# Kernel optimization log

Measured on AMD Instinct MI355X. Metric: run time of the kernel, lower is better.

Reference implementation:

```python
import jax, jax.numpy as jnp
import numpy as np

BLOCK_SIZE = 32
# E2M1 (FP4) representable magnitudes and rounding midpoints
FP4_GRID = jnp.array([0.0, 0.5, 1.0, 1.5, 2.0, 3.0, 4.0, 6.0], dtype=jnp.float32)
FP4_MIDS = jnp.array([0.25, 0.75, 1.25, 1.75, 2.5, 3.5, 5.0], dtype=jnp.float32)


def quantize_to_mxfp4(w, block_size=BLOCK_SIZE):
    """Quantize (K, N) weight to MXFP4: per-block-of-32 (along K) power-of-2 scale
    + E2M1 codes. Returns dequantized-code tensor q (K//bs, bs, N) and scales
    (K//bs, 1, N) so that dequant = q * scales."""
    K, N = w.shape
    wb = w.reshape(K // block_size, block_size, N)
    amax = jnp.max(jnp.abs(wb), axis=1, keepdims=True)          # (K//bs, 1, N)
    # E8M0 scale: 2^(floor(log2(amax)) - 2) so amax/scale falls in [4, 8) -> clipped to 6
    exp = jnp.floor(jnp.log2(jnp.maximum(amax, 1e-30))) - 2.0
    scales = jnp.exp2(exp)
    x = wb / scales
    idx = jnp.digitize(jnp.abs(x), FP4_MIDS)                    # round-to-nearest FP4 magnitude
    q = jnp.sign(x) * FP4_GRID[idx]
    return q, scales


def mxfp4_matmul(inputs, q, scales, block_size=BLOCK_SIZE):
    """inputs: (..., K); q: (K//bs, bs, N); scales: (K//bs, 1, N)."""
    K = inputs.shape[-1]
    N = q.shape[-1]
    w = (q * scales).reshape(K, N)   # fused dequant (reference form)
    return inputs @ w


def setup_inputs() -> dict:
    key = jax.random.key(0)
    ks = jax.random.split(key, 3)
    B, S, D, F = 4, 2048, 2048, 8192
    inputs = jax.random.normal(ks[0], (B, S, D), dtype=jnp.float32)
    up_kernel = jax.random.normal(ks[1], (D, F), dtype=jnp.float32) * (1.0 / np.sqrt(D))
    down_kernel = jax.random.normal(ks[2], (F, D), dtype=jnp.float32) * (1.0 / np.sqrt(F))
    up_bias = jnp.zeros((F,), dtype=jnp.float32)
    down_bias = jnp.zeros((D,), dtype=jnp.float32)
    return {"inputs": inputs, "up_kernel": up_kernel, "up_bias": up_bias,
            "down_kernel": down_kernel, "down_bias": down_bias}


def reference(inputs, up_kernel, up_bias, down_kernel, down_bias):
    q_up, s_up = quantize_to_mxfp4(up_kernel, BLOCK_SIZE)
    x = mxfp4_matmul(inputs, q_up, s_up, BLOCK_SIZE) + up_bias
    x = jax.nn.gelu(x)
    q_dn, s_dn = quantize_to_mxfp4(down_kernel, BLOCK_SIZE)
    x = mxfp4_matmul(x, q_dn, s_dn, BLOCK_SIZE) + down_bias
    return x
```

## Files before the change

### kernel.cpp

```cpp
#include <hip/hip_runtime.h>
#include <hip/hip_bf16.h>

typedef __bf16 bf16_t;
typedef __attribute__((ext_vector_type(8))) __bf16 bf16x8;
typedef __attribute__((ext_vector_type(4))) float f32x4;
typedef __attribute__((ext_vector_type(4))) unsigned int u32x4;

__device__ __forceinline__ void gload_lds16(const bf16_t* g, bf16_t* l) {
    __builtin_amdgcn_global_load_lds(
        (const __attribute__((address_space(1))) void*)g,
        (__attribute__((address_space(3))) void*)l,
        16, 0, 0);
}

__device__ __forceinline__ float gelu_f(float v) {
    float u = 0.7978845608028654f * (v + 0.044715f * v * v * v);
    float e = __expf(-2.f * u);
    float t = __fdividef(1.f - e, 1.f + e);
    return 0.5f * v * (1.f + t);
}

__device__ __forceinline__ void quant_one(const float* __restrict__ w,
                                          bf16_t* __restrict__ wt,
                                          int K, int N, int tix) {
    int n = tix % N;
    int b = tix / N;
    const float* src = w + (size_t)b * 32 * N + n;
    float v[32];
    float amax = 0.f;
#pragma unroll
    for (int i = 0; i < 32; ++i) {
        v[i] = __builtin_nontemporal_load(src + (size_t)i * N);
        amax = fmaxf(amax, fabsf(v[i]));
    }
    unsigned eb = (__float_as_uint(amax) >> 23) & 0xFF;
    float scale = __uint_as_float((eb - 2u) << 23);
    float inv   = __uint_as_float((256u - eb) << 23);
    if (amax == 0.f) { scale = 0.f; inv = 0.f; }
    bf16_t dq[32];
#pragma unroll
    for (int i = 0; i < 32; ++i) {
        float x  = v[i] * inv;
        float ax = fabsf(x);
        float q = ax < 0.25f ? 0.0f : ax < 0.75f ? 0.5f : ax < 1.25f ? 1.0f :
                  ax < 1.75f ? 1.5f : ax < 2.5f  ? 2.0f : ax < 3.5f  ? 3.0f :
                  ax < 5.0f  ? 4.0f : 6.0f;
        float d = copysignf(q * scale, x);
        dq[i] = (bf16_t)d;
    }
    const int r  = n & 255, rt = n >> 8, kt = b >> 1, ub = (b & 1) * 4;
    bf16_t* base = wt + (((size_t)rt * (K >> 6) + kt) << 14) + (r << 6);
#pragma unroll
    for (int j = 0; j < 4; ++j) {
        bf16x8 p;
#pragma unroll
        for (int t = 0; t < 8; ++t) p[t] = dq[j * 8 + t];
        *(bf16x8*)(base + (((ub + j) ^ (r & 7)) << 3)) = p;
    }
}

__global__ void prep_kernel(const float* __restrict__ in, bf16_t* __restrict__ out,
                            int ncvt, int cvtB, int dLog,
                            const float* __restrict__ upw, bf16_t* __restrict__ upwt,
                            int upK, int upN, int qupB,
                            const float* __restrict__ dnw, bf16_t* __restrict__ dnwt,
                            int dnK, int dnN) {
    int bid = blockIdx.x;
    if (bid < cvtB) {
        int i = (bid * blockDim.x + threadIdx.x) << 3;
        if (i >= ncvt) return;
        const f32x4* p = (const f32x4*)(in + i);
        f32x4 a = __builtin_nontemporal_load(p);
        f32x4 b = __builtin_nontemporal_load(p + 1);
        bf16x8 o;
        o[0] = (bf16_t)a[0]; o[1] = (bf16_t)a[1]; o[2] = (bf16_t)a[2]; o[3] = (bf16_t)a[3];
        o[4] = (bf16_t)b[0]; o[5] = (bf16_t)b[1]; o[6] = (bf16_t)b[2]; o[7] = (bf16_t)b[3];
        const int row = i >> dLog, d = i & ((1 << dLog) - 1);
        const int r = row & 255, mt = row >> 8, dt = d >> 6, u = (d >> 3) & 7;
        size_t off = (((size_t)mt * (1 << (dLog - 6)) + dt) << 14) + (r << 6)
                     + ((u ^ (r & 7)) << 3);
        *(bf16x8*)(out + off) = o;
    } else if (bid < cvtB + qupB) {
        int tix = (bid - cvtB) * blockDim.x + threadIdx.x;
        if (tix >= (upK >> 5) * upN) return;
        quant_one(upw, upwt, upK, upN, tix);
    } else {
        int tix = (bid - cvtB - qupB) * blockDim.x + threadIdx.x;
        if (tix >= (dnK >> 5) * dnN) return;
        quant_one(dnw, dnwt, dnK, dnN, tix);
    }
}

#define VMW4  asm volatile("s_waitcnt vmcnt(4)" ::: "memory")
#define VMW0  asm volatile("s_waitcnt vmcnt(0)" ::: "memory")
#define BARR  asm volatile("s_barrier" ::: "memory")
#define LGKM0 asm volatile("s_waitcnt lgkmcnt(0)" ::: "memory")

__global__ __launch_bounds__(512, 4)
void gemm1_kernel(const bf16_t* __restrict__ A, const bf16_t* __restrict__ Bt,
                  const float* __restrict__ bias, bf16_t* __restrict__ C,
                  int M, int N, int K) {
    __shared__ __align__(16) char smem[81920];
    bf16_t* sAp = (bf16_t*)smem;
    bf16_t* sBp = (bf16_t*)(smem + 65536);
    const int tid     = threadIdx.x;
    const int lane    = tid & 63;
    const int wv      = tid >> 6;
    const int wr      = wv >> 1;
    const int wc      = wv & 1;
    const int laneLow = lane & 15;
    const int laneHi  = lane >> 4;

    const int bid = blockIdx.x;
    const int xcd = bid & 7, l = bid >> 3, r = l >> 5, u = l & 31;
    const int bm = ((xcd & 1) << 3) + (u >> 2) + ((r & 1) << 4);
    const int bn = ((xcd >> 1) << 2) + (u & 3) + ((r >> 1) << 4);

    const int kT = K >> 6;
    const int rtB = bn >> 1;
    const size_t bHalf = (size_t)(bn & 1) << 13;

    auto stageA = [&](int buf, int kt) {
        const bf16_t* s = A + (((size_t)bm * kT + kt) << 14)
                            + ((wv * 8) << 6) + lane * 8;
        bf16_t* d = sAp + buf * 16384;
#pragma unroll
        for (int h = 0; h < 2; ++h) {
            gload_lds16(s + h * 8192,        d + (h * 128 + wv * 8) * 64);
            gload_lds16(s + h * 8192 + 4096, d + (h * 128 + 64 + wv * 8) * 64);
        }
    };
    auto stageB = [&](int kt) {
        const bf16_t* s = Bt + (((size_t)rtB * kT + kt) << 14) + bHalf
                             + ((wv * 8) << 6) + lane * 8;
        gload_lds16(s,        &sBp[(wv * 8) * 64]);
        gload_lds16(s + 4096, &sBp[(64 + wv * 8) * 64]);
    };

    const int s7  = laneLow & 7;
    const int xk0 = ((laneHi) ^ s7) << 3;
    const int xk1 = ((4 + laneHi) ^ s7) << 3;
    const int aOffBase = (wr * 64 + laneLow) * 64;
    const int bOffBase = (wc * 64 + laneLow) * 64;

    f32x4 acc[4][4];
#pragma unroll
    for (int i = 0; i < 4; ++i)
#pragma unroll
        for (int j = 0; j < 4; ++j) acc[i][j] = (f32x4){0.f, 0.f, 0.f, 0.f};

    stageA(0, 0);
    stageB(0);
    int cur = 0;

#pragma unroll 1
    for (int kt = 0; kt < kT; ++kt) {
        const bool nl = (kt + 1 < kT);
        if (nl) stageA(cur ^ 1, kt + 1);
        if (nl) { VMW4; } else { VMW0; }
        BARR;
        __builtin_amdgcn_s_setprio(1);
        const bf16_t* sAc = sAp + cur * 16384;
#pragma unroll
        for (int ks = 0; ks < 2; ++ks) {
            const int xk = ks ? xk1 : xk0;
            bf16x8 b0 = *(const bf16x8*)(&sBp[bOffBase + 0 * 1024 + xk]);
            bf16x8 b1 = *(const bf16x8*)(&sBp[bOffBase + 1 * 1024 + xk]);
            bf16x8 b2 = *(const bf16x8*)(&sBp[bOffBase + 2 * 1024 + xk]);
            bf16x8 b3 = *(const bf16x8*)(&sBp[bOffBase + 3 * 1024 + xk]);
#pragma unroll
            for (int m = 0; m < 4; ++m) {
                bf16x8 a = *(const bf16x8*)(&sAc[aOffBase + m * 1024 + xk]);
                acc[m][0] = __builtin_amdgcn_mfma_f32_16x16x32_bf16(a, b0, acc[m][0], 0, 0, 0);
                acc[m][1] = __builtin_amdgcn_mfma_f32_16x16x32_bf16(a, b1, acc[m][1], 0, 0, 0);
                acc[m][2] = __builtin_amdgcn_mfma_f32_16x16x32_bf16(a, b2, acc[m][2], 0, 0, 0);
                acc[m][3] = __builtin_amdgcn_mfma_f32_16x16x32_bf16(a, b3, acc[m][3], 0, 0, 0);
            }
        }
        __builtin_amdgcn_s_setprio(0);
        BARR;
        if (nl) stageB(kt + 1);
        cur ^= 1;
    }

    char* sC = smem;
#pragma unroll
    for (int n = 0; n < 4; ++n) {
        const int colL = wc * 64 + n * 16 + laneLow;
        const float bv = bias[bn * 128 + colL];
        const int u6   = (colL >> 3) & 7;
#pragma unroll
        for (int m = 0; m < 4; ++m) {
#pragma unroll
            for (int j = 0; j < 4; ++j) {
                const int rowL = wr * 64 + m * 16 + (laneHi << 2) + j;
                float v = acc[m][n][j] + bv;
                int byte = ((colL >> 6) << 15) + (rowL << 7)
                         + ((u6 ^ (rowL & 7)) << 4) + ((colL & 7) << 1);
                byte ^= ((rowL >> 2) & 3) << 5;
                *(bf16_t*)(sC + byte) = (bf16_t)gelu_f(v);
            }
        }
    }
    LGKM0;
    BARR;
    char* dst = (char*)C + (((size_t)bm * (N >> 6) + bn * 2) << 15);
#pragma unroll
    for (int s = 0; s < 8; ++s) {
        int lin = s * 8192 + tid * 16;
        int row = (lin >> 7) & 255;
        int rb  = lin ^ (((row >> 2) & 3) << 5);
        u32x4 v = *(const u32x4*)(sC + rb);
        __builtin_nontemporal_store(v, (u32x4*)(dst + lin));
    }
}

#define MFMA_ROW(MI, A0, A1)                                                          \
    acc[MI][0] = __builtin_amdgcn_mfma_f32_16x16x32_bf16(A0, bf00, acc[MI][0],0,0,0); \
    acc[MI][0] = __builtin_amdgcn_mfma_f32_16x16x32_bf16(A1, bf01, acc[MI][0],0,0,0); \
    acc[MI][1] = __builtin_amdgcn_mfma_f32_16x16x32_bf16(A0, bf10, acc[MI][1],0,0,0); \
    acc[MI][1] = __builtin_amdgcn_mfma_f32_16x16x32_bf16(A1, bf11, acc[MI][1],0,0,0); \
    acc[MI][2] = __builtin_amdgcn_mfma_f32_16x16x32_bf16(A0, bf20, acc[MI][2],0,0,0); \
    acc[MI][2] = __builtin_amdgcn_mfma_f32_16x16x32_bf16(A1, bf21, acc[MI][2],0,0,0); \
    acc[MI][3] = __builtin_amdgcn_mfma_f32_16x16x32_bf16(A0, bf30, acc[MI][3],0,0,0); \
    acc[MI][3] = __builtin_amdgcn_mfma_f32_16x16x32_bf16(A1, bf31, acc[MI][3],0,0,0);

#define PHASE(BUF, P, STAGE_STMT, TAIL_STMT)                                          \
  {                                                                                   \
    af00 = lda(BUF, 2*(P),   0); af01 = lda(BUF, 2*(P),   1);                         \
    af10 = lda(BUF, 2*(P)+1, 0); af11 = lda(BUF, 2*(P)+1, 1);                         \
    if ((P) == 0) {                                                                   \
      bf00 = ldb(BUF,0,0); bf01 = ldb(BUF,0,1);                                       \
      bf10 = ldb(BUF,1,0); bf11 = ldb(BUF,1,1);                                       \
      bf20 = ldb(BUF,2,0); bf21 = ldb(BUF,2,1);                                       \
      bf30 = ldb(BUF,3,0); bf31 = ldb(BUF,3,1);                                       \
    }                                                                                 \
    STAGE_STMT;                                                                       \
    BARR;                                                                             \
    LGKM0;                                                                            \
    __builtin_amdgcn_s_setprio(1);                                                    \
    MFMA_ROW(2*(P),   af00, af01);                                                    \
    MFMA_ROW(2*(P)+1, af10, af11);                                                    \
    __builtin_amdgcn_s_setprio(0);                                                    \
    TAIL_STMT;                                                                        \
    BARR;                                                                             \
  }

__global__ __launch_bounds__(512, 2)
void gemm2_kernel(const bf16_t* __restrict__ A, const bf16_t* __restrict__ Bt,
                  const float* __restrict__ bias, float* __restrict__ Cf,
                  int M, int N, int K) {
    __shared__ __align__(16) char smem[131072];
    bf16_t* sAp = (bf16_t*)smem;
    bf16_t* sBp = (bf16_t*)(smem + 65536);
    const int tid     = threadIdx.x;
    const int lane    = tid & 63;
    const int wv      = tid >> 6;
    const int wr      = wv >> 2;
    const int wc      = wv & 3;
    const int laneLow = lane & 15;
    const int laneHi  = lane >> 4;

    const int ntn = N >> 8;
    const int nwg = gridDim.x;
    const int bid = blockIdx.x;
    int wg  = (bid & 7) * (nwg >> 3) + (bid >> 3);
    const int bm = wg / ntn, bn = wg % ntn;

    const int kT = K >> 6;

    auto stageA = [&](int b, int kt, int h) {
        const bf16_t* s = A + (((size_t)bm * kT + kt) << 14)
                            + ((h * 128 + wv * 8) << 6) + lane * 8;
        gload_lds16(s,        &sAp[b * 16384 + (h * 128 + wv * 8) * 64]);
        gload_lds16(s + 4096, &sAp[b * 16384 + (h * 128 + 64 + wv * 8) * 64]);
    };
    auto stageB = [&](int b, int kt, int h) {
        const bf16_t* s = Bt + (((size_t)bn * kT + kt) << 14)
                             + ((h * 128 + wv * 8) << 6) + lane * 8;
        gload_lds16(s,        &sBp[b * 16384 + (h * 128 + wv * 8) * 64]);
        gload_lds16(s + 4096, &sBp[b * 16384 + (h * 128 + 64 + wv * 8) * 64]);
    };

    const int s7  = laneLow & 7;
    const int xk0 = ((laneHi) ^ s7) << 3;
    const int xk1 = ((4 + laneHi) ^ s7) << 3;
    const int aOffBase = (wr * 128 + laneLow) * 64;
    const int bOffBase = (wc * 64 + laneLow) * 64;
    auto lda = [&](int b, int m, int ks) -> bf16x8 {
        return *(const bf16x8*)(&sAp[b * 16384 + aOffBase + m * 1024 + (ks ? xk1 : xk0)]);
    };
    auto ldb = [&](int b, int n2, int ks) -> bf16x8 {
        return *(const bf16x8*)(&sBp[b * 16384 + bOffBase + n2 * 1024 + (ks ? xk1 : xk0)]);
    };

    f32x4 acc[8][4];
#pragma unroll
    for (int i = 0; i < 8; ++i)
#pragma unroll
        for (int j = 0; j < 4; ++j) acc[i][j] = (f32x4){0.f, 0.f, 0.f, 0.f};

    bf16x8 af00, af01, af10, af11;
    bf16x8 bf00, bf01, bf10, bf11, bf20, bf21, bf30, bf31;

    stageA(0, 0, 0); stageA(0, 0, 1);
    stageB(0, 0, 0); stageB(0, 0, 1);
    stageB(1, 1, 0); stageB(1, 1, 1);
    VMW4;
    BARR;

    const int niter = kT >> 1;
    for (int i = 0; i < niter; ++i) {
        const bool nlast = (i + 1 < niter);
        const int kO  = 2 * i + 1;
        const int kN  = 2 * i + 2;
        const int kN1 = 2 * i + 3;
        PHASE(0, 0, stageA(1, kO, 0), ((void)0));
        PHASE(0, 1, stageA(1, kO, 1), ((void)0));
        PHASE(0, 2, if (nlast) stageB(0, kN, 0), ((void)0));
        PHASE(0, 3, if (nlast) stageB(0, kN, 1),
              if (nlast) { VMW4; } else { VMW0; });
        PHASE(1, 0, if (nlast) stageA(0, kN, 0), ((void)0));
        PHASE(1, 1, if (nlast) stageA(0, kN, 1), ((void)0));
        PHASE(1, 2, if (nlast) stageB(1, kN1, 0), ((void)0));
        PHASE(1, 3, if (nlast) stageB(1, kN1, 1),
              if (nlast) { VMW4; });
    }

    const int r0 = bm * 256 + wr * 128 + (laneHi << 2);
    const int c0 = bn * 256 + wc * 64 + laneLow;
#pragma unroll
    for (int n = 0; n < 4; ++n) {
        const int col = c0 + n * 16;
        const float bv = bias[col];
#pragma unroll
        for (int m = 0; m < 8; ++m) {
#pragma unroll
            for (int j = 0; j < 4; ++j) {
                const int row = r0 + m * 16 + j;
                __builtin_nontemporal_store(acc[m][n][j] + bv,
                                            &Cf[(size_t)row * N + col]);
            }
        }
    }
}

extern "C" void kernel_launch(void* const* d_in, const int* in_sizes, int n_in,
                              void* d_out, int out_size, void* d_ws, size_t ws_size,
                              hipStream_t stream) {
    const float* inputs = (const float*)d_in[0];
    const float* up_w   = (const float*)d_in[1];
    const float* up_b   = (const float*)d_in[2];
    const float* dn_w   = (const float*)d_in[3];
    const float* dn_b   = (const float*)d_in[4];
    float* out = (float*)d_out;

    const int D = in_sizes[4];
    const int F = in_sizes[2];
    const int M = in_sizes[0] / D;
    const int dLog = 31 - __builtin_clz((unsigned)D);

    size_t r0_bytes = (size_t)(M > F ? M : F) * D * 2;
    char* ws = (char*)d_ws;
    bf16_t* in_bf = (bf16_t*)ws;
    bf16_t* wup_t = (bf16_t*)(ws + r0_bytes);
    bf16_t* mid   = (bf16_t*)(ws + r0_bytes + (size_t)F * D * 2);
    bf16_t* wdn_t = (bf16_t*)(ws + r0_bytes + (size_t)F * D * 2 + (size_t)M * F * 2);

    int ncvt = M * D;
    int cvtB = ncvt / (8 * 256);
    int qupB = ((D / 32) * F + 255) / 256;
    int qdnB = ((F / 32) * D + 255) / 256;
    prep_kernel<<<cvtB + qupB + qdnB, 256, 0, stream>>>(
        inputs, in_bf, ncvt, cvtB, dLog,
        up_w, wup_t, D, F, qupB,
        dn_w, wdn_t, F, D);

    gemm1_kernel<<<(M / 256) * (F / 128), 512, 0, stream>>>(
        in_bf, wup_t, up_b, mid, M, F, D);

    gemm2_kernel<<<(M / 256) * (D / 256), 512, 0, stream>>>(
        mid, wdn_t, dn_b, out, M, D, F);
    (void)ws_size; (void)n_in; (void)out_size;
}
```

Baseline: 542.6 us.

## Prefetch B tiles into registers two steps ahead in gemm1 main loop

Replaces the direct global-to-LDS load of the single-buffered B tile with register prefetch issued two k-tiles ahead. After the compute barrier, each thread writes the prefetched tile into LDS. The loop is unrolled by two with alternating register sets, and out-of-range tiles are clamped. The goal is to hide B load latency behind the MFMA phase instead of issuing the load only after the second barrier. It costs extra VGPRs, which may affect occupancy under launch_bounds(512,4), and adds redundant clamped loads at the tail. The loop assumes kT is even.

Result: no change. 535.2 us (-1.4%).

```diff
diff --git a/kernel.cpp b/kernel.cpp
--- a/kernel.cpp
+++ b/kernel.cpp
@@ -5,6 +5,7 @@
 typedef __attribute__((ext_vector_type(8))) __bf16 bf16x8;
 typedef __attribute__((ext_vector_type(4))) float f32x4;
 typedef __attribute__((ext_vector_type(4))) unsigned int u32x4;
+typedef const __attribute__((address_space(1))) u32x4* gbl_u32x4p;
 
 __device__ __forceinline__ void gload_lds16(const bf16_t* g, bf16_t* l) {
     __builtin_amdgcn_global_load_lds(
@@ -91,6 +92,7 @@
     }
 }
 
+#define VMW6  asm volatile("s_waitcnt vmcnt(6)" ::: "memory")
 #define VMW4  asm volatile("s_waitcnt vmcnt(4)" ::: "memory")
 #define VMW0  asm volatile("s_waitcnt vmcnt(0)" ::: "memory")
 #define BARR  asm volatile("s_barrier" ::: "memory")
@@ -120,6 +122,8 @@
     const int rtB = bn >> 1;
     const size_t bHalf = (size_t)(bn & 1) << 13;
 
+    auto cl = [&](int t) { return t < kT ? t : kT - 1; };
+
     auto stageA = [&](int buf, int kt) {
         const bf16_t* s = A + (((size_t)bm * kT + kt) << 14)
                             + ((wv * 8) << 6) + lane * 8;
@@ -130,11 +134,8 @@
             gload_lds16(s + h * 8192 + 4096, d + (h * 128 + 64 + wv * 8) * 64);
         }
     };
-    auto stageB = [&](int kt) {
-        const bf16_t* s = Bt + (((size_t)rtB * kT + kt) << 14) + bHalf
-                             + ((wv * 8) << 6) + lane * 8;
-        gload_lds16(s,        &sBp[(wv * 8) * 64]);
-        gload_lds16(s + 4096, &sBp[(64 + wv * 8) * 64]);
+    auto bsrc = [&](int kt) -> gbl_u32x4p {
+        return (gbl_u32x4p)(const void*)(Bt + (((size_t)rtB * kT + kt) << 14) + bHalf);
     };
 
     const int s7  = laneLow & 7;
@@ -149,39 +150,60 @@
 #pragma unroll
         for (int j = 0; j < 4; ++j) acc[i][j] = (f32x4){0.f, 0.f, 0.f, 0.f};
 
+    u32x4 rA0, rA1, rB0, rB1;
+
+    {
+        const bf16_t* s = Bt + (((size_t)rtB * kT) << 14) + bHalf
+                             + ((wv * 8) << 6) + lane * 8;
+        gload_lds16(s,        &sBp[(wv * 8) * 64]);
+        gload_lds16(s + 4096, &sBp[(64 + wv * 8) * 64]);
+    }
     stageA(0, 0);
-    stageB(0);
-    int cur = 0;
+    { gbl_u32x4p bs = bsrc(cl(1)); rA0 = bs[tid]; rA1 = bs[512 + tid]; }
+
+#define G1_MFMA(CUR)                                                              \
+    {                                                                             \
+        const bf16_t* sAc = sAp + (CUR) * 16384;                                  \
+        _Pragma("unroll")                                                         \
+        for (int ks = 0; ks < 2; ++ks) {                                          \
+            const int xk = ks ? xk1 : xk0;                                        \
+            bf16x8 b0 = *(const bf16x8*)(&sBp[bOffBase + 0 * 1024 + xk]);         \
+            bf16x8 b1 = *(const bf16x8*)(&sBp[bOffBase + 1 * 1024 + xk]);         \
+            bf16x8 b2 = *(const bf16x8*)(&sBp[bOffBase + 2 * 1024 + xk]);         \
+            bf16x8 b3 = *(const bf16x8*)(&sBp[bOffBase + 3 * 1024 + xk]);         \
+            _Pragma("unroll")                                                     \
+            for (int m = 0; m < 4; ++m) {                                         \
+                bf16x8 a = *(const bf16x8*)(&sAc[aOffBase + m * 1024 + xk]);      \
+                acc[m][0] = __builtin_amdgcn_mfma_f32_16x16x32_bf16(a, b0, acc[m][0], 0, 0, 0); \
+                acc[m][1] = __builtin_amdgcn_mfma_f32_16x16x32_bf16(a, b1, acc[m][1], 0, 0, 0); \
+                acc[m][2] = __builtin_amdgcn_mfma_f32_16x16x32_bf16(a, b2, acc[m][2], 0, 0, 0); \
+                acc[m][3] = __builtin_amdgcn_mfma_f32_16x16x32_bf16(a, b3, acc[m][3], 0, 0, 0); \
+            }                                                                     \
+        }                                                                         \
+    }
+
+#define G1_TILE(KT, CUR, LD0, LD1, WR0, WR1)                                      \
+    {                                                                             \
+        stageA((CUR) ^ 1, cl((KT) + 1));                                          \
+        { gbl_u32x4p bs = bsrc(cl((KT) + 2)); LD0 = bs[tid]; LD1 = bs[512 + tid]; } \
+        VMW6; LGKM0;                                                              \
+        BARR;                                                                     \
+        __builtin_amdgcn_s_setprio(1);                                            \
+        G1_MFMA(CUR);                                                             \
+        __builtin_amdgcn_s_setprio(0);                                            \
+        BARR;                                                                     \
+        ((u32x4*)sBp)[tid]       = WR0;                                           \
+        ((u32x4*)sBp)[512 + tid] = WR1;                                           \
+    }
 
 #pragma unroll 1
-    for (int kt = 0; kt < kT; ++kt) {
-        const bool nl = (kt + 1 < kT);
-        if (nl) stageA(cur ^ 1, kt + 1);
-        if (nl) { VMW4; } else { VMW0; }
-        BARR;
-        __builtin_amdgcn_s_setprio(1);
-        const bf16_t* sAc = sAp + cur * 16384;
-#pragma unroll
-        for (int ks = 0; ks < 2; ++ks) {
-            const int xk = ks ? xk1 : xk0;
-            bf16x8 b0 = *(const bf16x8*)(&sBp[bOffBase + 0 * 1024 + xk]);
-            bf16x8 b1 = *(const bf16x8*)(&sBp[bOffBase + 1 * 1024 + xk]);
-            bf16x8 b2 = *(const bf16x8*)(&sBp[bOffBase + 2 * 1024 + xk]);
-            bf16x8 b3 = *(const bf16x8*)(&sBp[bOffBase + 3 * 1024 + xk]);
-#pragma unroll
-            for (int m = 0; m < 4; ++m) {
-                bf16x8 a = *(const bf16x8*)(&sAc[aOffBase + m * 1024 + xk]);
-                acc[m][0] = __builtin_amdgcn_mfma_f32_16x16x32_bf16(a, b0, acc[m][0], 0, 0, 0);
-                acc[m][1] = __builtin_amdgcn_mfma_f32_16x16x32_bf16(a, b1, acc[m][1], 0, 0, 0);
-                acc[m][2] = __builtin_amdgcn_mfma_f32_16x16x32_bf16(a, b2, acc[m][2], 0, 0, 0);
-                acc[m][3] = __builtin_amdgcn_mfma_f32_16x16x32_bf16(a, b3, acc[m][3], 0, 0, 0);
-            }
-        }
-        __builtin_amdgcn_s_setprio(0);
-        BARR;
-        if (nl) stageB(kt + 1);
-        cur ^= 1;
-    }
+    for (int kp = 0; kp < (kT >> 1); ++kp) {
+        G1_TILE(2 * kp,     0, rB0, rB1, rA0, rA1);
+        G1_TILE(2 * kp + 1, 1, rA0, rA1, rB0, rB1);
+    }
+
+    VMW0; LGKM0;
+    BARR;
 
     char* sC = smem;
 #pragma unroll
```
